# Optimization experiments

Hardware: AMD Instinct MI355X
Metric: run time of the kernel (lower is better)

The kernel has to match this reference:

```python
import jax, jax.numpy as jnp
import numpy as np
import math

N_HEAD = 16
K_SPARSE = 64

def setup_inputs() -> dict:
    key = jax.random.key(0)
    ks = jax.random.split(key, 12)
    B, T, C = 1, 2048, 1024
    s = 0.02
    return {
        "x":   jax.random.normal(ks[0], (B, T, C), jnp.float32),
        "Wq":  jax.random.normal(ks[1], (C, C), jnp.float32) * s,
        "bq":  jax.random.normal(ks[2], (C,), jnp.float32) * s,
        "Wk":  jax.random.normal(ks[3], (C, C), jnp.float32) * s,
        "bk":  jax.random.normal(ks[4], (C,), jnp.float32) * s,
        "Wv":  jax.random.normal(ks[5], (C, C), jnp.float32) * s,
        "bv":  jax.random.normal(ks[6], (C,), jnp.float32) * s,
        "Wo":  jax.random.normal(ks[7], (C, C), jnp.float32) * s,
        "bo":  jax.random.normal(ks[8], (C,), jnp.float32) * s,
        "Wks": jax.random.normal(ks[9], (C,), jnp.float32) * s,
        "bks": jax.random.normal(ks[10], (), jnp.float32) * s,
    }

def reference(x, Wq, bq, Wk, bk, Wv, bv, Wo, bo, Wks, bks):
    B, T, C = x.shape
    nh = N_HEAD
    hs = C // nh
    k_val = min(K_SPARSE, T)

    # projections -> (B, nh, T, hs)   (torch Linear: x @ W.T + b)
    q = (x @ Wq.T + bq).reshape(B, T, nh, hs).transpose(0, 2, 1, 3)
    k = (x @ Wk.T + bk).reshape(B, T, nh, hs).transpose(0, 2, 1, 3)
    v = (x @ Wv.T + bv).reshape(B, T, nh, hs).transpose(0, 2, 1, 3)

    # key scorer: per-token scalar score (B, T)
    key_scores = x @ Wks + bks

    # causal masking of scores, then per-query top-k key selection
    pos = jnp.arange(T)
    causal = pos[None, :] <= pos[:, None]                      # (T, T), True where key<=query
    masked = jnp.where(causal[None], key_scores[:, None, :], -jnp.inf)  # (B, T, T)
    _, top_k_idx = jax.lax.top_k(masked, k_val)                # (B, T, k)
    top_k_idx = jnp.minimum(top_k_idx, pos[None, :, None])     # clamp to <= query pos

    # gather sparse keys/values: (B, nh, T, k, hs)
    bi = jnp.arange(B)[:, None, None, None]
    hi = jnp.arange(nh)[None, :, None, None]
    gi = top_k_idx[:, None, :, :]                              # (B, 1, T, k)
    sparse_k = k[bi, hi, gi]                                   # (B, nh, T, k, hs)
    sparse_v = v[bi, hi, gi]

    scale = 1.0 / math.sqrt(hs)
    logits = jnp.einsum('bhtd,bhtkd->bhtk', q, sparse_k) * scale
    probs = jax.nn.softmax(logits, axis=-1)
    out = jnp.einsum('bhtk,bhtkd->bhtd', probs, sparse_v)      # (B, nh, T, hs)
    out = out.transpose(0, 2, 1, 3).reshape(B, T, C)
    return out @ Wo.T + bo
```

## Files before the change

kernel.cpp:

```cpp
#include <hip/hip_runtime.h>
#include <hip/hip_bf16.h>
#include <cstdint>
#include <cstddef>

#define T_DIM 2048
#define C_DIM 1024
#define NH 16
#define HS 64
#define KSP 64

#define QBM 128
#define QBN 128
#define QBK 64
#define OBM 64
#define OBN 64
#define GBK 128

#define ATB 16
#define VTS 102
#define PLS 96

typedef short short8 __attribute__((ext_vector_type(8)));
typedef float f32x4 __attribute__((ext_vector_type(4)));
typedef _Float16 half8 __attribute__((ext_vector_type(8)));

__device__ __forceinline__ unsigned short f2bfu(float f) {
  unsigned u = __builtin_bit_cast(unsigned, f);
  unsigned r = (u + 0x7fffu + ((u >> 16) & 1u)) >> 16;
  return (unsigned short)r;
}
__device__ __forceinline__ unsigned short f2h(float f) {
  _Float16 h = (_Float16)f;
  return __builtin_bit_cast(unsigned short, h);
}

#define GLOAD_LDS16(gp, lp)                                                  \
  __builtin_amdgcn_global_load_lds(                                          \
      (const __attribute__((address_space(1))) void*)(gp),                   \
      (__attribute__((address_space(3))) void*)(lp), 16, 0, 0)

#define NSCORE (T_DIM / 4)
#define NCONV ((T_DIM * C_DIM + 4 * C_DIM * C_DIM) / 4 / 256)
__global__ __launch_bounds__(256) void convert_scores_kernel(
    const float* __restrict__ x, const float* __restrict__ Wq,
    const float* __restrict__ Wk, const float* __restrict__ Wv,
    const float* __restrict__ Wo, const float* __restrict__ Wks,
    const float* __restrict__ bks,
    unsigned short* __restrict__ xb, unsigned short* __restrict__ Wqb,
    unsigned short* __restrict__ Wkb, unsigned short* __restrict__ Wvb,
    unsigned short* __restrict__ Wob, float* __restrict__ scores) {
  if (blockIdx.x < NSCORE) {
    const int t = blockIdx.x * 4 + (threadIdx.x >> 6);
    const int lane = threadIdx.x & 63;
    const float* xrow = x + (size_t)t * C_DIM;
    float acc = 0.f;
    #pragma unroll 4
    for (int i = lane; i < C_DIM; i += 64)
      acc += xrow[i] * Wks[i];
    #pragma unroll
    for (int o = 32; o; o >>= 1) acc += __shfl_xor(acc, o);
    if (lane == 0) scores[t] = acc + bks[0];
    return;
  }
  const int i = (blockIdx.x - NSCORE) * 256 + threadIdx.x;
  const int NX4 = T_DIM * C_DIM / 4;
  const int NW4 = C_DIM * C_DIM / 4;
  const float* src;
  unsigned short* dst;
  int j = i;
  if (j < NX4) { src = x; dst = xb; }
  else {
    j -= NX4;
    int w = j / NW4;
    j -= w * NW4;
    src = (w == 0) ? Wq : (w == 1) ? Wk : (w == 2) ? Wv : Wo;
    dst = (w == 0) ? Wqb : (w == 1) ? Wkb : (w == 2) ? Wvb : Wob;
  }
  float4 f = reinterpret_cast<const float4*>(src)[j];
  ushort4 o;
  o.x = f2bfu(f.x); o.y = f2bfu(f.y); o.z = f2bfu(f.z); o.w = f2bfu(f.w);
  reinterpret_cast<ushort4*>(dst)[j] = o;
}

__device__ __forceinline__ void gemm_body_128x128(
    const unsigned short* __restrict__ A, const unsigned short* __restrict__ W,
    f32x4 acc[4][4], int bm, int bn, int tid,
    unsigned short* As, unsigned short* Ws) {
  const int w = tid >> 6, lane = tid & 63;
  const int quad = lane >> 4, r = lane & 15;
  const int wm = (w >> 1) * 64, wn = (w & 1) * 64;
  const int sub8 = lane >> 3;
  const int c8 = lane & 7;
  const unsigned short* Arow[4];
  const unsigned short* Wrow[4];
  #pragma unroll
  for (int i = 0; i < 4; ++i) {
    const int row = i * 32 + w * 8 + sub8;
    Arow[i] = A + (size_t)(bm * QBM + row) * C_DIM + ((c8 ^ (row & 7)) * 8);
    Wrow[i] = W + (size_t)(bn * QBN + row) * C_DIM + ((c8 ^ (row & 7)) * 8);
  }
  for (int kb = 0; kb < C_DIM; kb += QBK) {
    #pragma unroll
    for (int i = 0; i < 4; ++i)
      GLOAD_LDS16(Arow[i] + kb, &As[(i * 32 + w * 8) * QBK]);
    #pragma unroll
    for (int i = 0; i < 4; ++i)
      GLOAD_LDS16(Wrow[i] + kb, &Ws[(i * 32 + w * 8) * QBK]);
    __syncthreads();
    #pragma unroll
    for (int ks = 0; ks < 2; ++ks) {
      const int pc = ((ks * 4 + quad) ^ (r & 7)) * 8;
      short8 af[4], bfr[4];
      #pragma unroll
      for (int mi = 0; mi < 4; ++mi)
        af[mi] = *reinterpret_cast<const short8*>(&As[(wm + mi * 16 + r) * QBK + pc]);
      #pragma unroll
      for (int ni = 0; ni < 4; ++ni)
        bfr[ni] = *reinterpret_cast<const short8*>(&Ws[(wn + ni * 16 + r) * QBK + pc]);
      #pragma unroll
      for (int mi = 0; mi < 4; ++mi)
        #pragma unroll
        for (int ni = 0; ni < 4; ++ni)
          acc[mi][ni] = __builtin_amdgcn_mfma_f32_16x16x32_bf16(af[mi], bfr[ni], acc[mi][ni], 0, 0, 0);
    }
    __syncthreads();
  }
}

#define NRANK (T_DIM / 4)
#define QPER ((T_DIM / QBM) * (C_DIM / QBN))
__global__ __launch_bounds__(256) void gemm_qkv_rank_kernel(
    const unsigned short* __restrict__ A,
    const unsigned short* __restrict__ Wq, const unsigned short* __restrict__ Wk,
    const unsigned short* __restrict__ Wv,
    const float* __restrict__ bq, const float* __restrict__ bk,
    const float* __restrict__ bv,
    unsigned short* __restrict__ qo, unsigned short* __restrict__ ko,
    unsigned short* __restrict__ vo,
    const float* __restrict__ scores, int* __restrict__ sorted_idx) {
  __shared__ unsigned short lds[2 * QBM * QBK];
  const int tid = threadIdx.x;
  if (blockIdx.x < NRANK) {
    float* ss = reinterpret_cast<float*>(lds);
    for (int j = tid; j < T_DIM; j += 256) ss[j] = scores[j];
    __syncthreads();
    const int w = tid >> 6, lane = tid & 63;
    const int i = blockIdx.x * 4 + w;
    const float si = ss[i];
    int rank = 0;
    #pragma unroll
    for (int step = 0; step < T_DIM / 64; ++step) {
      const int j = step * 64 + lane;
      const float sj = ss[j];
      rank += (int)((sj > si) || (sj == si && j < i));
    }
    #pragma unroll
    for (int o = 32; o; o >>= 1) rank += __shfl_xor(rank, o);
    if (lane == 0) sorted_idx[rank] = i;
    return;
  }
  const int bid = blockIdx.x - NRANK;
  const int which = bid / QPER;
  const int rem = bid % QPER;
  const int bm = rem / (C_DIM / QBN);
  const int bn = rem % (C_DIM / QBN);
  const unsigned short* W = (which == 0) ? Wq : (which == 1) ? Wk : Wv;
  const float* bias = (which == 0) ? bq : (which == 1) ? bk : bv;
  unsigned short* out = (which == 0) ? qo : (which == 1) ? ko : vo;
  f32x4 acc[4][4] = {};
  gemm_body_128x128(A, W, acc, bm, bn, tid, lds, lds + QBM * QBK);
  const int w = tid >> 6, lane = tid & 63;
  const int quad = lane >> 4, r = lane & 15;
  const int wm = (w >> 1) * 64, wn = (w & 1) * 64;
  #pragma unroll
  for (int mi = 0; mi < 4; ++mi) {
    #pragma unroll
    for (int ni = 0; ni < 4; ++ni) {
      const int col = bn * QBN + wn + ni * 16 + r;
      const float bf = bias[col];
      #pragma unroll
      for (int i = 0; i < 4; ++i) {
        const int row = bm * QBM + wm + mi * 16 + quad * 4 + i;
        const float val = acc[mi][ni][i] + bf;
        out[(size_t)row * C_DIM + col] = f2h(val);
      }
    }
  }
}

__device__ __forceinline__ void gemm_body_64x64(
    const unsigned short* __restrict__ A, const unsigned short* __restrict__ W,
    f32x4 acc[2][2], int bm, int bn, int tid) {
  __shared__ unsigned short As[OBM * GBK];
  __shared__ unsigned short Ws[OBN * GBK];
  const int w = tid >> 6, lane = tid & 63;
  const int quad = lane >> 4, r = lane & 15;
  const int wm = (w >> 1) * 32, wn = (w & 1) * 32;
  const int sub = lane >> 4;
  const int c = lane & 15;
  const unsigned short* Arow[4];
  const unsigned short* Wrow[4];
  #pragma unroll
  for (int i = 0; i < 4; ++i) {
    const int row = w * 16 + i * 4 + sub;
    Arow[i] = A + (size_t)(bm * OBM + row) * C_DIM + ((c ^ (row & 7)) * 8);
    Wrow[i] = W + (size_t)(bn * OBN + row) * C_DIM + ((c ^ (row & 7)) * 8);
  }
  for (int kb = 0; kb < C_DIM; kb += GBK) {
    #pragma unroll
    for (int i = 0; i < 4; ++i)
      GLOAD_LDS16(Arow[i] + kb, &As[(w * 16 + i * 4) * GBK]);
    #pragma unroll
    for (int i = 0; i < 4; ++i)
      GLOAD_LDS16(Wrow[i] + kb, &Ws[(w * 16 + i * 4) * GBK]);
    __syncthreads();
    #pragma unroll
    for (int ks = 0; ks < 4; ++ks) {
      const int pc = ((ks * 4 + quad) ^ (r & 7)) * 8;
      short8 af[2], bfr[2];
      #pragma unroll
      for (int mi = 0; mi < 2; ++mi)
        af[mi] = *reinterpret_cast<const short8*>(&As[(wm + mi * 16 + r) * GBK + pc]);
      #pragma unroll
      for (int ni = 0; ni < 2; ++ni)
        bfr[ni] = *reinterpret_cast<const short8*>(&Ws[(wn + ni * 16 + r) * GBK + pc]);
      #pragma unroll
      for (int mi = 0; mi < 2; ++mi)
        #pragma unroll
        for (int ni = 0; ni < 2; ++ni)
          acc[mi][ni] = __builtin_amdgcn_mfma_f32_16x16x32_bf16(af[mi], bfr[ni], acc[mi][ni], 0, 0, 0);
    }
    __syncthreads();
  }
}

__global__ __launch_bounds__(256) void gemm_o_f32_kernel(
    const unsigned short* __restrict__ A, const unsigned short* __restrict__ W,
    const float* __restrict__ bias, float* __restrict__ out) {
  const int tid = threadIdx.x;
  const int bm = blockIdx.x / (C_DIM / OBN);
  const int bn = blockIdx.x % (C_DIM / OBN);
  f32x4 acc[2][2] = {};
  gemm_body_64x64(A, W, acc, bm, bn, tid);
  const int w = tid >> 6, lane = tid & 63;
  const int quad = lane >> 4, r = lane & 15;
  const int wm = (w >> 1) * 32, wn = (w & 1) * 32;
  #pragma unroll
  for (int mi = 0; mi < 2; ++mi) {
    #pragma unroll
    for (int ni = 0; ni < 2; ++ni) {
      const int col = bn * OBN + wn + ni * 16 + r;
      const float bf = bias[col];
      #pragma unroll
      for (int i = 0; i < 4; ++i) {
        const int row = bm * OBM + wm + mi * 16 + quad * 4 + i;
        out[(size_t)row * C_DIM + col] = acc[mi][ni][i] + bf;
      }
    }
  }
}

__global__ __launch_bounds__(256) void select_kernel(
    const int* __restrict__ sorted_idx, unsigned short* __restrict__ sel) {
  const int tid = threadIdx.x;
  const int w = tid >> 6, lane = tid & 63;
  const int t = blockIdx.x * 4 + w;
  unsigned short* dst = sel + (size_t)t * KSP;
  if (t <= 63) {
    dst[lane] = (unsigned short)((lane < t) ? lane : t);
    return;
  }
  const unsigned long long lt_mask = (1ull << lane) - 1ull;
  int count = 0;
  for (int c = 0; c < T_DIM / 64 && count < KSP; ++c) {
    int s = sorted_idx[c * 64 + lane];
    s = (s < 0) ? 0 : (s > T_DIM - 1 ? T_DIM - 1 : s);
    const bool ok = (s <= t);
    const unsigned long long mm = __ballot(ok);
    const int pos = count + __popcll(mm & lt_mask);
    if (ok && pos < KSP) dst[pos] = (unsigned short)s;
    count += __popcll(mm);
  }
}

__global__ __launch_bounds__(128) void attn_kernel(
    const unsigned short* __restrict__ q, const unsigned short* __restrict__ k,
    const unsigned short* __restrict__ v, const unsigned short* __restrict__ sel,
    unsigned short* __restrict__ attn_out) {
  __shared__ __align__(16) unsigned char arena[32416];
  unsigned short* VtB = reinterpret_cast<unsigned short*>(arena);
  unsigned short* PlB = reinterpret_cast<unsigned short*>(arena + 26112);
  unsigned char* map8 = arena + 26112;
  unsigned char* cnt8 = arena + 26112 + 2048;
  unsigned short* urows = reinterpret_cast<unsigned short*>(arena + 32256);
  const int tb = blockIdx.x >> 3;
  const int hg = blockIdx.x & 7;
  const int t0 = tb * ATB;
  const int tid = threadIdx.x;
  const int w = tid >> 6, lane = tid & 63;
  const int qd = lane >> 4;
  const int r = lane & 15;
  const int h = hg * 2 + w;
  unsigned short* Vtw = VtB + w * 64 * VTS;
  unsigned short* Plw = PlB + w * 16 * PLS;

  uint4 qf[2];
  #pragma unroll
  for (int kc = 0; kc < 2; ++kc)
    qf[kc] = *reinterpret_cast<const uint4*>(
        q + (size_t)(t0 + r) * C_DIM + h * HS + kc * 32 + qd * 8);

  if (tid < KSP) {
    const int r0 = sel[(size_t)t0 * KSP + tid];
    urows[tid] = (unsigned short)r0;
    if (t0 >= 64) map8[r0] = (unsigned char)tid;
  } else if (tid < 79) {
    const int row = t0 + 1 + (tid - KSP);
    urows[tid] = (unsigned short)row;
    if (t0 >= 64) map8[row] = (unsigned char)tid;
  } else if (tid == 79) {
    urows[79] = (unsigned short)t0;
  }
  if (t0 >= 64) {
    for (int i = tid; i < 320; i += 128)
      reinterpret_cast<unsigned*>(cnt8)[i] = 0u;
  }
  __syncthreads();

  uint4 kf[5][2];
  #pragma unroll
  for (int ut = 0; ut < 5; ++ut) {
    const int rowg = urows[ut * 16 + r];
    const unsigned short* kr = k + (size_t)rowg * C_DIM + h * HS + qd * 8;
    kf[ut][0] = *reinterpret_cast<const uint4*>(kr);
    kf[ut][1] = *reinterpret_cast<const uint4*>(kr + 32);
  }

  {
    const int e8 = lane & 7;
    const int pr = lane >> 3;
    #pragma unroll
    for (int sb = 0; sb < 5; ++sb) {
      const int s0 = sb * 16 + pr * 2;
      const int row0 = urows[s0], row1 = urows[s0 + 1];
      const size_t g0 = (size_t)row0 * C_DIM + h * HS + e8 * 8;
      const size_t g1 = (size_t)row1 * C_DIM + h * HS + e8 * 8;
      const uint4 v0 = *reinterpret_cast<const uint4*>(v + g0);
      const uint4 v1 = *reinterpret_cast<const uint4*>(v + g1);
      const unsigned* v0w = reinterpret_cast<const unsigned*>(&v0);
      const unsigned* v1w = reinterpret_cast<const unsigned*>(&v1);
      #pragma unroll
      for (int dd = 0; dd < 8; ++dd) {
        const unsigned lo = (v0w[dd >> 1] >> ((dd & 1) * 16)) & 0xffffu;
        const unsigned hi = (v1w[dd >> 1] >> ((dd & 1) * 16)) & 0xffffu;
        *reinterpret_cast<unsigned*>(&Vtw[(e8 * 8 + dd) * VTS + s0]) =
            lo | (hi << 16);
      }
    }
    #pragma unroll
    for (int z = 0; z < 8; ++z)
      *reinterpret_cast<unsigned*>(&Vtw[lane * VTS + 80 + z * 2]) = 0u;
    if (t0 >= 64) {
      #pragma unroll
      for (int e = 0; e < 8; ++e) {
        const int idx = tid + e * 128;
        const int tl = idx >> 6;
        const int rr = sel[(size_t)(t0 + tl) * KSP + (idx & 63)];
        cnt8[tl * 80 + map8[rr]] = 1;
      }
    } else if (tid < 80) {
      const int s = tid;
      #pragma unroll
      for (int tl = 0; tl < ATB; ++tl) {
        const int t = t0 + tl;
        int c;
        if (s < t0)        c = 1;
        else if (s == t0)  c = (tl == 0) ? (64 - t) : 1;
        else if (s < 64)   c = 0;
        else if (s < 79) {
          const int row = t0 + 1 + (s - 64);
          c = (row < t) ? 1 : ((row == t) ? (64 - t) : 0);
        } else c = 0;
        cnt8[tl * 80 + s] = (unsigned char)c;
      }
    }
  }
  __syncthreads();

  f32x4 s5[5] = {};
  #pragma unroll
  for (int ut = 0; ut < 5; ++ut) {
    #pragma unroll
    for (int kc = 0; kc < 2; ++kc) {
      s5[ut] = __builtin_amdgcn_mfma_f32_16x16x32_f16(
          __builtin_bit_cast(half8, kf[ut][kc]), __builtin_bit_cast(half8, qf[kc]),
          s5[ut], 0, 0, 0);
    }
  }
  float mx = -3.0e38f;
  #pragma unroll
  for (int ut = 0; ut < 5; ++ut) {
    const unsigned c4 =
        *reinterpret_cast<const unsigned*>(cnt8 + r * 80 + ut * 16 + qd * 4);
    #pragma unroll
    for (int i = 0; i < 4; ++i) {
      const unsigned cc = (c4 >> (8 * i)) & 0xffu;
      float lg = s5[ut][i] * 0.125f;
      lg = (cc == 0u) ? -3.0e38f
         : (cc == 1u) ? lg : (lg + __logf((float)cc));
      s5[ut][i] = lg;
      mx = fmaxf(mx, lg);
    }
  }
  mx = fmaxf(mx, __shfl_xor(mx, 16));
  mx = fmaxf(mx, __shfl_xor(mx, 32));
  float sum = 0.f;
  #pragma unroll
  for (int ut = 0; ut < 5; ++ut)
    #pragma unroll
    for (int i = 0; i < 4; ++i) {
      const float e = __expf(s5[ut][i] - mx);
      s5[ut][i] = e;
      sum += e;
    }
  sum += __shfl_xor(sum, 16);
  sum += __shfl_xor(sum, 32);
  const float rs = 1.0f / sum;
  __syncthreads();
  #pragma unroll
  for (int ut = 0; ut < 5; ++ut) {
    const unsigned w0 = (unsigned)f2h(s5[ut][0] * rs) |
                        ((unsigned)f2h(s5[ut][1] * rs) << 16);
    const unsigned w1 = (unsigned)f2h(s5[ut][2] * rs) |
                        ((unsigned)f2h(s5[ut][3] * rs) << 16);
    unsigned* p32 = reinterpret_cast<unsigned*>(&Plw[r * PLS + ut * 16 + qd * 4]);
    p32[0] = w0;
    p32[1] = w1;
  }
  *reinterpret_cast<unsigned long long*>(&Plw[r * PLS + 80 + qd * 4]) = 0ull;
  f32x4 o4[4] = {};
  #pragma unroll
  for (int c = 0; c < 3; ++c) {
    const uint4 pw = *reinterpret_cast<const uint4*>(&Plw[r * PLS + c * 32 + qd * 8]);
    #pragma unroll
    for (int mt = 0; mt < 4; ++mt) {
      const unsigned short* vb_ = &Vtw[(mt * 16 + r) * VTS + c * 32 + qd * 8];
      uint4 vw;
      vw.x = *reinterpret_cast<const unsigned*>(vb_);
      vw.y = *reinterpret_cast<const unsigned*>(vb_ + 2);
      vw.z = *reinterpret_cast<const unsigned*>(vb_ + 4);
      vw.w = *reinterpret_cast<const unsigned*>(vb_ + 6);
      o4[mt] = __builtin_amdgcn_mfma_f32_16x16x32_f16(
          __builtin_bit_cast(half8, vw), __builtin_bit_cast(half8, pw),
          o4[mt], 0, 0, 0);
    }
  }
  #pragma unroll
  for (int mt = 0; mt < 4; ++mt) {
    ushort4 ov;
    ov.x = f2bfu(o4[mt][0]); ov.y = f2bfu(o4[mt][1]);
    ov.z = f2bfu(o4[mt][2]); ov.w = f2bfu(o4[mt][3]);
    *reinterpret_cast<ushort4*>(
        attn_out + (size_t)(t0 + r) * C_DIM + h * HS + mt * 16 + qd * 4) = ov;
  }
}

extern "C" void kernel_launch(void* const* d_in, const int* in_sizes, int n_in,
                              void* d_out, int out_size, void* d_ws, size_t ws_size,
                              hipStream_t stream) {
  const float* x   = (const float*)d_in[0];
  const float* Wq  = (const float*)d_in[1];
  const float* bq  = (const float*)d_in[2];
  const float* Wk  = (const float*)d_in[3];
  const float* bk  = (const float*)d_in[4];
  const float* Wv  = (const float*)d_in[5];
  const float* bv  = (const float*)d_in[6];
  const float* Wo  = (const float*)d_in[7];
  const float* bo  = (const float*)d_in[8];
  const float* Wks = (const float*)d_in[9];
  const float* bks = (const float*)d_in[10];
  float* out = (float*)d_out;

  char* ws = (char*)d_ws;
  size_t off = 0;
  float* scores = (float*)(ws + off); off += 8192;
  int*   sorted = (int*)(ws + off);   off += 8192;
  unsigned short* selb = (unsigned short*)(ws + off); off += (size_t)T_DIM * KSP * 2;
  unsigned short* xb  = (unsigned short*)(ws + off); off += (size_t)T_DIM * C_DIM * 2;
  unsigned short* Wqb = (unsigned short*)(ws + off); off += (size_t)C_DIM * C_DIM * 2;
  unsigned short* Wkb = (unsigned short*)(ws + off); off += (size_t)C_DIM * C_DIM * 2;
  unsigned short* Wvb = (unsigned short*)(ws + off); off += (size_t)C_DIM * C_DIM * 2;
  unsigned short* Wob = (unsigned short*)(ws + off); off += (size_t)C_DIM * C_DIM * 2;
  unsigned short* qb  = (unsigned short*)(ws + off); off += (size_t)T_DIM * C_DIM * 2;
  unsigned short* kb  = (unsigned short*)(ws + off); off += (size_t)T_DIM * C_DIM * 2;
  unsigned short* vb  = (unsigned short*)(ws + off); off += (size_t)T_DIM * C_DIM * 2;
  unsigned short* ab  = xb;

  convert_scores_kernel<<<NSCORE + NCONV, 256, 0, stream>>>(
      x, Wq, Wk, Wv, Wo, Wks, bks, xb, Wqb, Wkb, Wvb, Wob, scores);

  gemm_qkv_rank_kernel<<<NRANK + 3 * QPER, 256, 0, stream>>>(
      xb, Wqb, Wkb, Wvb, bq, bk, bv, qb, kb, vb, scores, sorted);

  select_kernel<<<T_DIM / 4, 256, 0, stream>>>(sorted, selb);

  attn_kernel<<<(T_DIM / ATB) * (NH / 2), 128, 0, stream>>>(qb, kb, vb, selb, ab);

  gemm_o_f32_kernel<<<(T_DIM / OBM) * (C_DIM / OBN), 256, 0, stream>>>(
      ab, Wob, bo, out);
}
```

Before: 146.5 us.

## Fuse Q/K/V projections into one tile sharing the A block across three weights

Replaces the separate 128x128 tiles for each of Q, K and V with one 128x32 output tile per block that loads the x tile once and multiplies it against matching 32-column slices of Wq, Wk and Wv. The goal is to cut redundant reads of the activation tile and to raise the block count from 384 to 512 for better occupancy. In exchange, each warp computes a smaller 32x32 tile per weight, so arithmetic intensity per LDS load drops and more synchronizations run per unit of work.

```diff
diff --git a/kernel.cpp b/kernel.cpp
--- a/kernel.cpp
+++ b/kernel.cpp
@@ -9,9 +9,10 @@
 #define HS 64
 #define KSP 64
 
-#define QBM 128
-#define QBN 128
-#define QBK 64
+#define FBM 128
+#define FBN 32
+#define FBK 64
+#define FPER ((T_DIM / FBM) * (C_DIM / FBN))
 #define OBM 64
 #define OBN 64
 #define GBK 128
@@ -82,53 +83,7 @@
   reinterpret_cast<ushort4*>(dst)[j] = o;
 }
 
-__device__ __forceinline__ void gemm_body_128x128(
-    const unsigned short* __restrict__ A, const unsigned short* __restrict__ W,
-    f32x4 acc[4][4], int bm, int bn, int tid,
-    unsigned short* As, unsigned short* Ws) {
-  const int w = tid >> 6, lane = tid & 63;
-  const int quad = lane >> 4, r = lane & 15;
-  const int wm = (w >> 1) * 64, wn = (w & 1) * 64;
-  const int sub8 = lane >> 3;
-  const int c8 = lane & 7;
-  const unsigned short* Arow[4];
-  const unsigned short* Wrow[4];
-  #pragma unroll
-  for (int i = 0; i < 4; ++i) {
-    const int row = i * 32 + w * 8 + sub8;
-    Arow[i] = A + (size_t)(bm * QBM + row) * C_DIM + ((c8 ^ (row & 7)) * 8);
-    Wrow[i] = W + (size_t)(bn * QBN + row) * C_DIM + ((c8 ^ (row & 7)) * 8);
-  }
-  for (int kb = 0; kb < C_DIM; kb += QBK) {
-    #pragma unroll
-    for (int i = 0; i < 4; ++i)
-      GLOAD_LDS16(Arow[i] + kb, &As[(i * 32 + w * 8) * QBK]);
-    #pragma unroll
-    for (int i = 0; i < 4; ++i)
-      GLOAD_LDS16(Wrow[i] + kb, &Ws[(i * 32 + w * 8) * QBK]);
-    __syncthreads();
-    #pragma unroll
-    for (int ks = 0; ks < 2; ++ks) {
-      const int pc = ((ks * 4 + quad) ^ (r & 7)) * 8;
-      short8 af[4], bfr[4];
-      #pragma unroll
-      for (int mi = 0; mi < 4; ++mi)
-        af[mi] = *reinterpret_cast<const short8*>(&As[(wm + mi * 16 + r) * QBK + pc]);
-      #pragma unroll
-      for (int ni = 0; ni < 4; ++ni)
-        bfr[ni] = *reinterpret_cast<const short8*>(&Ws[(wn + ni * 16 + r) * QBK + pc]);
-      #pragma unroll
-      for (int mi = 0; mi < 4; ++mi)
-        #pragma unroll
-        for (int ni = 0; ni < 4; ++ni)
-          acc[mi][ni] = __builtin_amdgcn_mfma_f32_16x16x32_bf16(af[mi], bfr[ni], acc[mi][ni], 0, 0, 0);
-    }
-    __syncthreads();
-  }
-}
-
 #define NRANK (T_DIM / 4)
-#define QPER ((T_DIM / QBM) * (C_DIM / QBN))
 __global__ __launch_bounds__(256) void gemm_qkv_rank_kernel(
     const unsigned short* __restrict__ A,
     const unsigned short* __restrict__ Wq, const unsigned short* __restrict__ Wk,
@@ -138,7 +93,7 @@
     unsigned short* __restrict__ qo, unsigned short* __restrict__ ko,
     unsigned short* __restrict__ vo,
     const float* __restrict__ scores, int* __restrict__ sorted_idx) {
-  __shared__ unsigned short lds[2 * QBM * QBK];
+  __shared__ unsigned short lds[FBM * FBK + 3 * FBN * FBK];
   const int tid = threadIdx.x;
   if (blockIdx.x < NRANK) {
     float* ss = reinterpret_cast<float*>(lds);
@@ -160,29 +115,91 @@
     return;
   }
   const int bid = blockIdx.x - NRANK;
-  const int which = bid / QPER;
-  const int rem = bid % QPER;
-  const int bm = rem / (C_DIM / QBN);
-  const int bn = rem % (C_DIM / QBN);
-  const unsigned short* W = (which == 0) ? Wq : (which == 1) ? Wk : Wv;
-  const float* bias = (which == 0) ? bq : (which == 1) ? bk : bv;
-  unsigned short* out = (which == 0) ? qo : (which == 1) ? ko : vo;
-  f32x4 acc[4][4] = {};
-  gemm_body_128x128(A, W, acc, bm, bn, tid, lds, lds + QBM * QBK);
+  const int bm = bid >> 5;
+  const int bn = bid & 31;
   const int w = tid >> 6, lane = tid & 63;
   const int quad = lane >> 4, r = lane & 15;
-  const int wm = (w >> 1) * 64, wn = (w & 1) * 64;
-  #pragma unroll
-  for (int mi = 0; mi < 4; ++mi) {
-    #pragma unroll
-    for (int ni = 0; ni < 4; ++ni) {
-      const int col = bn * QBN + wn + ni * 16 + r;
-      const float bf = bias[col];
-      #pragma unroll
-      for (int i = 0; i < 4; ++i) {
-        const int row = bm * QBM + wm + mi * 16 + quad * 4 + i;
-        const float val = acc[mi][ni][i] + bf;
-        out[(size_t)row * C_DIM + col] = f2h(val);
+  const int sub8 = lane >> 3, c8 = lane & 7;
+  unsigned short* As = lds;
+  unsigned short* Ws0 = lds + FBM * FBK;
+  unsigned short* Ws1 = Ws0 + FBN * FBK;
+  unsigned short* Ws2 = Ws1 + FBN * FBK;
+  const unsigned short* Arow[4];
+  #pragma unroll
+  for (int i = 0; i < 4; ++i) {
+    const int row = i * 32 + w * 8 + sub8;
+    Arow[i] = A + (size_t)(bm * FBM + row) * C_DIM + ((c8 ^ (row & 7)) * 8);
+  }
+  const int wrow = w * 8 + sub8;
+  const size_t woff = (size_t)(bn * FBN + wrow) * C_DIM + ((c8 ^ (wrow & 7)) * 8);
+  f32x4 acc[3][2][2] = {};
+  for (int kb = 0; kb < C_DIM; kb += FBK) {
+    #pragma unroll
+    for (int i = 0; i < 4; ++i)
+      GLOAD_LDS16(Arow[i] + kb, &As[(i * 32 + w * 8) * FBK]);
+    GLOAD_LDS16(Wq + woff + kb, &Ws0[(w * 8) * FBK]);
+    GLOAD_LDS16(Wk + woff + kb, &Ws1[(w * 8) * FBK]);
+    GLOAD_LDS16(Wv + woff + kb, &Ws2[(w * 8) * FBK]);
+    __syncthreads();
+    #pragma unroll
+    for (int ks = 0; ks < 2; ++ks) {
+      const int pc = ((ks * 4 + quad) ^ (r & 7)) * 8;
+      short8 af[2];
+      #pragma unroll
+      for (int mi = 0; mi < 2; ++mi)
+        af[mi] = *reinterpret_cast<const short8*>(&As[(w * 32 + mi * 16 + r) * FBK + pc]);
+      {
+        short8 bfr[2];
+        #pragma unroll
+        for (int ni = 0; ni < 2; ++ni)
+          bfr[ni] = *reinterpret_cast<const short8*>(&Ws0[(ni * 16 + r) * FBK + pc]);
+        #pragma unroll
+        for (int mi = 0; mi < 2; ++mi)
+          #pragma unroll
+          for (int ni = 0; ni < 2; ++ni)
+            acc[0][mi][ni] = __builtin_amdgcn_mfma_f32_16x16x32_bf16(af[mi], bfr[ni], acc[0][mi][ni], 0, 0, 0);
+      }
+      {
+        short8 bfr[2];
+        #pragma unroll
+        for (int ni = 0; ni < 2; ++ni)
+          bfr[ni] = *reinterpret_cast<const short8*>(&Ws1[(ni * 16 + r) * FBK + pc]);
+        #pragma unroll
+        for (int mi = 0; mi < 2; ++mi)
+          #pragma unroll
+          for (int ni = 0; ni < 2; ++ni)
+            acc[1][mi][ni] = __builtin_amdgcn_mfma_f32_16x16x32_bf16(af[mi], bfr[ni], acc[1][mi][ni], 0, 0, 0);
+      }
+      {
+        short8 bfr[2];
+        #pragma unroll
+        for (int ni = 0; ni < 2; ++ni)
+          bfr[ni] = *reinterpret_cast<const short8*>(&Ws2[(ni * 16 + r) * FBK + pc]);
+        #pragma unroll
+        for (int mi = 0; mi < 2; ++mi)
+          #pragma unroll
+          for (int ni = 0; ni < 2; ++ni)
+            acc[2][mi][ni] = __builtin_amdgcn_mfma_f32_16x16x32_bf16(af[mi], bfr[ni], acc[2][mi][ni], 0, 0, 0);
+      }
+    }
+    __syncthreads();
+  }
+  const int wm = w * 32;
+  #pragma unroll
+  for (int j = 0; j < 3; ++j) {
+    const float* bias = (j == 0) ? bq : (j == 1) ? bk : bv;
+    unsigned short* out = (j == 0) ? qo : (j == 1) ? ko : vo;
+    #pragma unroll
+    for (int mi = 0; mi < 2; ++mi) {
+      #pragma unroll
+      for (int ni = 0; ni < 2; ++ni) {
+        const int col = bn * FBN + ni * 16 + r;
+        const float bf = bias[col];
+        #pragma unroll
+        for (int i = 0; i < 4; ++i) {
+          const int row = bm * FBM + wm + mi * 16 + quad * 4 + i;
+          out[(size_t)row * C_DIM + col] = f2h(acc[j][mi][ni][i] + bf);
+        }
       }
     }
   }
@@ -499,7 +516,7 @@
   convert_scores_kernel<<<NSCORE + NCONV, 256, 0, stream>>>(
       x, Wq, Wk, Wv, Wo, Wks, bks, xb, Wqb, Wkb, Wvb, Wob, scores);
 
-  gemm_qkv_rank_kernel<<<NRANK + 3 * QPER, 256, 0, stream>>>(
+  gemm_qkv_rank_kernel<<<NRANK + FPER, 256, 0, stream>>>(
       xb, Wqb, Wkb, Wvb, bq, bk, bv, qb, kb, vb, scores, sorted);
 
   select_kernel<<<T_DIM / 4, 256, 0, stream>>>(sorted, selb);
```

New measurement: 143.7 us (median of 2 runs). About the same (-1.9%).
